# Kernel tuning notes

Hardware: AMD Instinct MI355X
Metric: run time of the kernel (lower is better)

Reference implementation:

```python
import jax, jax.numpy as jnp
import numpy as np

K = 8          # opt.pk, explicit precision cutoff
MARGIN = 0.2   # opt.margin
NEG = -1e30    # sentinel for masked sort keys


def setup_inputs() -> dict:
    key = jax.random.key(0)
    k1, k2 = jax.random.split(key)
    batch_reprs = jax.random.normal(k1, (4096, 512), dtype=jnp.float32)
    batch_labels = jax.random.randint(k2, (4096,), 0, 64)
    return {"batch_reprs": batch_reprs, "batch_labels": batch_labels}


def _forward(batch_reprs, batch_labels):
    B = batch_reprs.shape[0]
    dt = batch_reprs.dtype
    # cls_match_mat: 1 if same class
    match = (batch_labels[:, None] == batch_labels[None, :]).astype(dt)
    # pairwise euclidean distance (squared=False), safe sqrt at zero diagonal
    sq = jnp.sum(batch_reprs * batch_reprs, axis=1)
    res = jnp.maximum(sq[:, None] - 2.0 * (batch_reprs @ batch_reprs.T) + sq[None, :], 0.0)
    zero = res <= 0.0
    d = jnp.where(zero, 0.0, jnp.sqrt(jnp.where(zero, 1.0, res)))
    sim_hat = -d + (1.0 - match) * MARGIN  # use_margin=True path
    # rank via double argsort (descending similarity -> rank 1 = best)
    order = jnp.argsort(-sim_hat, axis=1)
    rank = jnp.argsort(order, axis=1).astype(dt) + 1.0
    pos_nums = jnp.sum(match, axis=1)
    ks = jnp.minimum(pos_nums, jnp.asarray(K + 1, dt))[:, None]  # k_mat per row
    w = 1.0 / jnp.log2(rank + 1.0) + 1.0  # DCG-style rank weight
    # false positives: not same class, within top-k_i
    fp_mask = (match < 1.0) & (rank <= ks)
    fp_nums = jnp.sum(fp_mask, axis=1)  # |N| per row
    # false negatives: same class, beyond top-k_i
    fn_mask = (match > 0.0) & (rank > ks)
    fp_term = jnp.sum(jnp.where(fp_mask, sim_hat * w, 0.0))
    # per-row variable-size topk over false negatives, vectorized:
    # mask non-FN entries to -inf, sort desc, keep first fp_nums[i] entries
    fn_key = jnp.where(fn_mask, sim_hat, NEG)
    fn_order = jnp.argsort(-fn_key, axis=1)
    sorted_sim = jnp.take_along_axis(sim_hat, fn_order, axis=1)
    sorted_w = jnp.take_along_axis(w, fn_order, axis=1)
    sorted_valid = jnp.take_along_axis(fn_mask, fn_order, axis=1)
    take = (jnp.arange(B)[None, :].astype(dt) < fp_nums[:, None]) & sorted_valid
    fn_term = jnp.sum(jnp.where(take, sorted_sim * sorted_w, 0.0))
    # rows with fp_num==0 contribute 0 to both terms, matching the host loop
    return fp_term - fn_term


def reference(batch_reprs, batch_labels):
    return _forward(batch_reprs, batch_labels)
```

## Files before the change

### kernel.cpp

```cpp
#include <hip/hip_runtime.h>
#include <math.h>

#define BB 4096
#define DD 512
#define KTOP 9
#define MARGIN_F 0.2f
#define NT64 64
#define NTRI64 (NT64 * (NT64 + 1) / 2)

typedef __attribute__((ext_vector_type(8))) short short8;
typedef __attribute__((ext_vector_type(4))) float f32x4;
typedef unsigned long long u64;

__device__ unsigned short g_Rhi[(size_t)BB * DD];
__device__ unsigned short g_Rlo[(size_t)BB * DD];
__device__ u64 g_cmask[64 * 64];

__device__ __forceinline__ unsigned short f2bf(float x) {
  unsigned u = __float_as_uint(x);
  u += 0x7fffu + ((u >> 16) & 1u);
  return (unsigned short)(u >> 16);
}
__device__ __forceinline__ float bf2f(unsigned short h) {
  return __uint_as_float((unsigned)h << 16);
}

__device__ __forceinline__ void gload16(void* lds, const void* g) {
  __builtin_amdgcn_global_load_lds(
      (const __attribute__((address_space(1))) void*)g,
      (__attribute__((address_space(3))) void*)lds, 16, 0, 0);
}

#define FENCE() asm volatile("" ::: "memory")

__device__ __forceinline__ float ord16val(unsigned o16) {
  unsigned e = (o16 << 16) | 0x8000u;
  unsigned s = (e & 0x80000000u) ? (e ^ 0x80000000u) : ~e;
  return __uint_as_float(s);
}

__device__ __forceinline__ unsigned wavemax32_dpp(unsigned c) {
#define MSTEP(CTRL, RM)                                                        \
  {                                                                            \
    unsigned o = (unsigned)__builtin_amdgcn_update_dpp(0, (int)c, CTRL, RM, 0xf, false); \
    if (o > c) c = o;                                                          \
  }
  MSTEP(0xB1, 0xf) MSTEP(0x4E, 0xf) MSTEP(0x141, 0xf) MSTEP(0x140, 0xf)
  MSTEP(0x142, 0xa) MSTEP(0x143, 0xc)
#undef MSTEP
  return (unsigned)__builtin_amdgcn_readlane((int)c, 63);
}

__device__ __forceinline__ int wavesum_dpp(int c) {
#define SSTEP(CTRL, RM)                                                        \
  c += __builtin_amdgcn_update_dpp(0, c, CTRL, RM, 0xf, false);
  SSTEP(0xB1, 0xf) SSTEP(0x4E, 0xf) SSTEP(0x141, 0xf) SSTEP(0x140, 0xf)
  SSTEP(0x142, 0xa) SSTEP(0x143, 0xc)
#undef SSTEP
  return __builtin_amdgcn_readlane(c, 63);
}

__device__ __forceinline__ unsigned u4c(const uint4& f, int q) {
  return q == 0 ? f.x : q == 1 ? f.y : q == 2 ? f.z : f.w;
}

__global__ __launch_bounds__(64) void splitsq(const float* __restrict__ R,
                                              float* __restrict__ sq) {
  const int row = blockIdx.x, lane = threadIdx.x;
  const float4* r4 = (const float4*)(R + (size_t)row * DD);
  float4 a = r4[lane], b = r4[lane + 64];
  float xs[8] = {a.x, a.y, a.z, a.w, b.x, b.y, b.z, b.w};
  unsigned short hs[8], ls[8];
  float s = 0.f;
  #pragma unroll
  for (int q = 0; q < 8; ++q) {
    float x = xs[q];
    s += x * x;
    unsigned short hh = f2bf(x);
    hs[q] = hh;
    ls[q] = f2bf(x - bf2f(hh));
  }
  const size_t base = (size_t)row * DD;
  *(ushort4*)&g_Rhi[base + lane * 4]       = *(ushort4*)&hs[0];
  *(ushort4*)&g_Rhi[base + 256 + lane * 4] = *(ushort4*)&hs[4];
  *(ushort4*)&g_Rlo[base + lane * 4]       = *(ushort4*)&ls[0];
  *(ushort4*)&g_Rlo[base + 256 + lane * 4] = *(ushort4*)&ls[4];
  #pragma unroll
  for (int off = 32; off; off >>= 1) s += __shfl_down(s, off);
  if (lane == 0) sq[row] = s;
}

__global__ __launch_bounds__(64) void buildmask(const int* __restrict__ labels) {
  __shared__ int slab[BB];
  const int c = blockIdx.x, lane = threadIdx.x;
  for (int i = lane; i < BB / 4; i += 64) ((int4*)slab)[i] = ((const int4*)labels)[i];
  __syncthreads();
  u64 m = 0;
  #pragma unroll
  for (int e = 0; e < 64; ++e) {
    int j = 512 * (e >> 3) + 8 * lane + (e & 7);
    m |= (u64)(slab[j] == c) << e;
  }
  g_cmask[c * 64 + lane] = m;
}

__global__ __launch_bounds__(256) void simgemm_mfma(const int* __restrict__ labels,
                                                    const float* __restrict__ sq,
                                                    unsigned short* __restrict__ simq) {
  const int x = blockIdx.x & 7;
  int c = blockIdx.x >> 3;
  int bi = 0, bj = 0;
  #pragma unroll
  for (int q = 0; q < 8; ++q) {
    const int bjq = (q < 4) ? (4 * x + q) : (56 - 4 * x + q);
    const int n = bjq + 1;
    if (c >= 0 && c < n) { bj = bjq; bi = c; }
    c -= n;
  }
  const int i0 = bi * 64, j0 = bj * 64;

  __shared__ unsigned short smem[3][3 * 2048];

  const int tid = threadIdx.x;
  const int wid = tid >> 6, lane = tid & 63;
  const int wr = wid >> 1, wc = wid & 1;
  const int lrow = lane & 15, kblk = lane >> 4;

  const int r_a = lane >> 2;
  const int c_sw = (((lane & 3) ^ (r_a & 3)) * 8);

  f32x4 acc[2][2] = {};

  auto stage = [&](unsigned short* buf, int k0) {
    const int r = wid * 16 + r_a;
    const size_t ga = (size_t)(i0 + r) * DD + k0 + c_sw;
    const size_t gb = (size_t)(j0 + r) * DD + k0 + c_sw;
    gload16(&buf[wid * 512],        &g_Rhi[ga]);
    gload16(&buf[2048 + wid * 512], &g_Rhi[gb]);
    gload16(&buf[4096 + wid * 512], &g_Rlo[gb]);
  };

  stage(smem[0], 0);
  stage(smem[1], 32);

  #pragma unroll
  for (int step = 0; step < 16; ++step) {
    if (step + 2 < 16) stage(smem[(step + 2) % 3], (step + 2) * 32);
    if (step < 14)      asm volatile("s_waitcnt vmcnt(6)" ::: "memory");
    else if (step == 14) asm volatile("s_waitcnt vmcnt(3)" ::: "memory");
    else                 asm volatile("s_waitcnt vmcnt(0)" ::: "memory");
    __builtin_amdgcn_s_barrier();
    FENCE();

    unsigned short* sAhi = smem[step % 3];
    unsigned short* sBhi = sAhi + 2048;
    unsigned short* sBlo = sAhi + 4096;

    short8 ah[2], bh[2], bl[2];
    #pragma unroll
    for (int m = 0; m < 2; ++m) {
      const int rr = wr * 32 + m * 16 + lrow;
      const int off = rr * 32 + ((kblk ^ (lrow & 3)) * 8);
      ah[m] = *(const short8*)&sAhi[off];
    }
    #pragma unroll
    for (int n = 0; n < 2; ++n) {
      const int rr = wc * 32 + n * 16 + lrow;
      const int off = rr * 32 + ((kblk ^ (lrow & 3)) * 8);
      bh[n] = *(const short8*)&sBhi[off];
      bl[n] = *(const short8*)&sBlo[off];
    }
    #pragma unroll
    for (int m = 0; m < 2; ++m) {
      #pragma unroll
      for (int n = 0; n < 2; ++n) {
        acc[m][n] = __builtin_amdgcn_mfma_f32_16x16x32_bf16(ah[m], bh[n], acc[m][n], 0, 0, 0);
        acc[m][n] = __builtin_amdgcn_mfma_f32_16x16x32_bf16(ah[m], bl[n], acc[m][n], 0, 0, 0);
      }
    }
    FENCE();
    __builtin_amdgcn_s_barrier();
    FENCE();
  }

  __syncthreads();
  unsigned short (*T)[68] = (unsigned short (*)[68])smem[0];
  float* sqi = (float*)smem[1];
  float* sqj = sqi + 64;
  int* labi = (int*)(sqj + 64);
  int* labj = labi + 64;
  if (tid < 64) { sqi[tid] = sq[i0 + tid]; labi[tid] = labels[i0 + tid]; }
  else if (tid < 128) { int t2 = tid - 64; sqj[t2] = sq[j0 + t2]; labj[t2] = labels[j0 + t2]; }
  __syncthreads();

  #pragma unroll
  for (int m = 0; m < 2; ++m) {
    const int rbase = wr * 32 + m * 16 + kblk * 4;
    #pragma unroll
    for (int n = 0; n < 2; ++n) {
      const int ccol = wc * 32 + n * 16 + lrow;
      const float sqc = sqj[ccol];
      const int lc_ = labj[ccol];
      #pragma unroll
      for (int reg = 0; reg < 4; ++reg) {
        const int r = rbase + reg;
        float res = sqi[r] - 2.0f * acc[m][n][reg] + sqc;
        float dd = (res <= 0.f) ? 0.f : sqrtf(res);
        float sv = -dd + ((labi[r] != lc_) ? MARGIN_F : 0.f);
        unsigned su = __float_as_uint(sv);
        unsigned ord = su ^ ((unsigned)((int)su >> 31) | 0x80000000u);
        T[r][ccol] = (unsigned short)(ord >> 16);
      }
    }
  }
  __syncthreads();

  const bool offdiag = (bi != bj);
  const int row = tid >> 2, seg = tid & 3;
  uint4 w0 = *(const uint4*)&T[row][seg * 16];
  uint4 w1 = *(const uint4*)&T[row][seg * 16 + 8];
  *(uint4*)&simq[(size_t)(i0 + row) * BB + j0 + seg * 16]     = w0;
  *(uint4*)&simq[(size_t)(i0 + row) * BB + j0 + seg * 16 + 8] = w1;
  if (offdiag) {
    unsigned short tmp[16];
    #pragma unroll
    for (int r2 = 0; r2 < 16; ++r2) tmp[r2] = T[seg * 16 + r2][row];
    *(uint4*)&simq[(size_t)(j0 + row) * BB + i0 + seg * 16]     = *(uint4*)&tmp[0];
    *(uint4*)&simq[(size_t)(j0 + row) * BB + i0 + seg * 16 + 8] = *(uint4*)&tmp[8];
  }
}

#define EKEY(e) ((((u4c(v[(e) >> 3], ((e) & 7) >> 1) >> (16 * ((e) & 1))) & 0xffffu) << 13) \
                 | (lbase - (unsigned)((512 * ((e) >> 3) + ((e) & 7)) << 1)                 \
                    + (unsigned)((mask >> (e)) & 1ull)))

#define TOP2UPD(k, a, b) {                                                     \
  unsigned _mx = ((k) > (a)) ? (k) : (a);                                      \
  unsigned _mn = ((k) > (a)) ? (a) : (k);                                      \
  (a) = _mx;                                                                   \
  (b) = (_mn > (b)) ? _mn : (b); }

__global__ __launch_bounds__(256) void rowproc6(const unsigned short* __restrict__ simq,
                                                const int* __restrict__ labels,
                                                float* __restrict__ partials) {
  const int tid = threadIdx.x;
  const int lane = tid & 63;
  const int row = blockIdx.x * 4 + (tid >> 6);

  const uint4* rowp = (const uint4*)(simq + (size_t)row * BB);
  uint4 v[8];
  #pragma unroll
  for (int s = 0; s < 8; ++s) v[s] = rowp[lane + s * 64];

  const int myl = labels[row];
  const u64 mask = g_cmask[myl * 64 + lane];
  const unsigned lbase = (unsigned)((4095 - 8 * lane) << 1);

  unsigned h1 = 0, h2 = 0;
  #pragma unroll
  for (int e = 0; e < 64; ++e) {
    unsigned k = EKEY(e);
    TOP2UPD(k, h1, h2);
  }
  const int pos = wavesum_dpp(__popcll(mask));
  const int ks = min(pos, KTOP);

  unsigned kth = 0;
  float fp = 0.f; int fpn = 0;
  #pragma unroll
  for (int t = 0; t < KTOP; ++t) {
    if (t < ks) {
      unsigned g = wavemax32_dpp(h1);
      if (!(g & 1u)) { fp += ord16val(g >> 13) * (1.f / log2f((float)(t + 2)) + 1.f); fpn++; }
      if (t == ks - 1) kth = g;
      if (h1 == g) {
        h1 = h2; h2 = ~0u;
        if (h1 == ~0u) {
          h1 = 0; h2 = 0;
          #pragma unroll
          for (int e = 0; e < 64; ++e) {
            unsigned k = EKEY(e);
            if (k < g) TOP2UPD(k, h1, h2);
          }
        }
      }
    }
  }

  float fn = 0.f;
  if (fpn > 0) {
    unsigned f1 = 0, f2 = 0;
    #pragma unroll
    for (int e = 0; e < 64; ++e) {
      unsigned k = EKEY(e);
      if ((k & 1u) && k < kth) TOP2UPD(k, f1, f2);
    }
    unsigned ck[KTOP];
    int nc = 0;
    #pragma unroll
    for (int u = 0; u < KTOP; ++u) {
      ck[u] = ~0u;
      if (u < fpn) {
        unsigned g = wavemax32_dpp(f1);
        if (g != 0u) {
          ck[u] = g; nc = u + 1;
          if (f1 == g) {
            f1 = f2; f2 = ~0u;
            if (f1 == ~0u) {
              f1 = 0; f2 = 0;
              #pragma unroll
              for (int e = 0; e < 64; ++e) {
                unsigned k = EKEY(e);
                if ((k & 1u) && k < g) TOP2UPD(k, f1, f2);
              }
            }
          }
        }
      }
    }
    if (nc > 0) {
      int cnt[KTOP];
      #pragma unroll
      for (int u = 0; u < KTOP; ++u) cnt[u] = 0;
      #pragma unroll
      for (int e = 0; e < 64; ++e) {
        unsigned k = EKEY(e);
        #pragma unroll
        for (int u = 0; u < KTOP; ++u) cnt[u] += (k > ck[u]) ? 1 : 0;
      }
      #pragma unroll
      for (int u = 0; u < KTOP; ++u) cnt[u] = wavesum_dpp(cnt[u]);
      #pragma unroll
      for (int u = 0; u < KTOP; ++u) {
        if (u < nc) {
          int rank = 1 + cnt[u];
          fn += ord16val(ck[u] >> 13) * (1.f / log2f((float)(rank + 1)) + 1.f);
        }
      }
    }
  }

  if (lane == 0) partials[row] = fp - fn;
}

__global__ __launch_bounds__(256) void finalreduce(const float* __restrict__ partials,
                                                   float* __restrict__ out) {
  __shared__ float s[256];
  const int tid = threadIdx.x;
  float acc = 0.f;
  for (int j = tid; j < BB; j += 256) acc += partials[j];
  s[tid] = acc; __syncthreads();
  #pragma unroll
  for (int st = 128; st; st >>= 1) { if (tid < st) s[tid] += s[tid + st]; __syncthreads(); }
  if (tid == 0) out[0] = s[0];
}

extern "C" void kernel_launch(void* const* d_in, const int* in_sizes, int n_in,
                              void* d_out, int out_size, void* d_ws, size_t ws_size,
                              hipStream_t stream) {
  const float* R      = (const float*)d_in[0];
  const int*   labels = (const int*)d_in[1];
  float* out = (float*)d_out;

  unsigned short* simq = (unsigned short*)d_ws;
  float* sq            = (float*)((char*)d_ws + (size_t)BB * BB * 2);
  float* partials      = sq + BB;

  splitsq<<<BB, 64, 0, stream>>>(R, sq);
  buildmask<<<64, 64, 0, stream>>>(labels);
  simgemm_mfma<<<NTRI64, 256, 0, stream>>>(labels, sq, simq);
  rowproc6<<<BB / 4, 256, 0, stream>>>(simq, labels, partials);
  finalreduce<<<1, 256, 0, stream>>>(partials, out);
}
```

Baseline: 97.56 us.

## Drop bf16 low-part split GEMM and use single-wave 64x64 tiles

Removes the hi/lo bf16 split of the B operand, so the distance GEMM runs in plain bf16 with half the MFMA work and no g_Rlo writes or reads. The GEMM kernel is rebuilt as one wave per 64x64 tile with a 4x4 accumulator grid, double-buffered LDS loads, and no block barriers. The epilogue transpose and stores are redone for 64 threads. Lower precision can change the similarity ordering near ties and so shift ranks, and fewer threads per block lowers per-block parallelism and epilogue throughput.

```diff
diff --git a/kernel.cpp b/kernel.cpp
--- a/kernel.cpp
+++ b/kernel.cpp
@@ -13,7 +13,6 @@
 typedef unsigned long long u64;
 
 __device__ unsigned short g_Rhi[(size_t)BB * DD];
-__device__ unsigned short g_Rlo[(size_t)BB * DD];
 __device__ u64 g_cmask[64 * 64];
 
 __device__ __forceinline__ unsigned short f2bf(float x) {
@@ -21,17 +20,12 @@
   u += 0x7fffu + ((u >> 16) & 1u);
   return (unsigned short)(u >> 16);
 }
-__device__ __forceinline__ float bf2f(unsigned short h) {
-  return __uint_as_float((unsigned)h << 16);
-}
 
 __device__ __forceinline__ void gload16(void* lds, const void* g) {
   __builtin_amdgcn_global_load_lds(
       (const __attribute__((address_space(1))) void*)g,
       (__attribute__((address_space(3))) void*)lds, 16, 0, 0);
 }
-
-#define FENCE() asm volatile("" ::: "memory")
 
 __device__ __forceinline__ float ord16val(unsigned o16) {
   unsigned e = (o16 << 16) | 0x8000u;
@@ -70,21 +64,17 @@
   const float4* r4 = (const float4*)(R + (size_t)row * DD);
   float4 a = r4[lane], b = r4[lane + 64];
   float xs[8] = {a.x, a.y, a.z, a.w, b.x, b.y, b.z, b.w};
-  unsigned short hs[8], ls[8];
+  unsigned short hs[8];
   float s = 0.f;
   #pragma unroll
   for (int q = 0; q < 8; ++q) {
     float x = xs[q];
     s += x * x;
-    unsigned short hh = f2bf(x);
-    hs[q] = hh;
-    ls[q] = f2bf(x - bf2f(hh));
+    hs[q] = f2bf(x);
   }
   const size_t base = (size_t)row * DD;
   *(ushort4*)&g_Rhi[base + lane * 4]       = *(ushort4*)&hs[0];
   *(ushort4*)&g_Rhi[base + 256 + lane * 4] = *(ushort4*)&hs[4];
-  *(ushort4*)&g_Rlo[base + lane * 4]       = *(ushort4*)&ls[0];
-  *(ushort4*)&g_Rlo[base + 256 + lane * 4] = *(ushort4*)&ls[4];
   #pragma unroll
   for (int off = 32; off; off >>= 1) s += __shfl_down(s, off);
   if (lane == 0) sq[row] = s;
@@ -104,9 +94,9 @@
   g_cmask[c * 64 + lane] = m;
 }
 
-__global__ __launch_bounds__(256) void simgemm_mfma(const int* __restrict__ labels,
-                                                    const float* __restrict__ sq,
-                                                    unsigned short* __restrict__ simq) {
+__global__ __launch_bounds__(64) void simgemm_wave(const int* __restrict__ labels,
+                                                   const float* __restrict__ sq,
+                                                   unsigned short* __restrict__ simq) {
   const int x = blockIdx.x & 7;
   int c = blockIdx.x >> 3;
   int bi = 0, bj = 0;
@@ -119,86 +109,69 @@
   }
   const int i0 = bi * 64, j0 = bj * 64;
 
-  __shared__ unsigned short smem[3][3 * 2048];
-
-  const int tid = threadIdx.x;
-  const int wid = tid >> 6, lane = tid & 63;
-  const int wr = wid >> 1, wc = wid & 1;
+  __shared__ unsigned short smem[2][2][2048];
+
+  const int lane = threadIdx.x;
   const int lrow = lane & 15, kblk = lane >> 4;
 
-  const int r_a = lane >> 2;
-  const int c_sw = (((lane & 3) ^ (r_a & 3)) * 8);
-
-  f32x4 acc[2][2] = {};
-
-  auto stage = [&](unsigned short* buf, int k0) {
-    const int r = wid * 16 + r_a;
-    const size_t ga = (size_t)(i0 + r) * DD + k0 + c_sw;
-    const size_t gb = (size_t)(j0 + r) * DD + k0 + c_sw;
-    gload16(&buf[wid * 512],        &g_Rhi[ga]);
-    gload16(&buf[2048 + wid * 512], &g_Rhi[gb]);
-    gload16(&buf[4096 + wid * 512], &g_Rlo[gb]);
+  f32x4 acc[4][4] = {};
+
+  auto stage = [&](int buf, int k0) {
+    const int sr = lane & 15;
+    const int sc = (lane >> 4) * 8;
+    #pragma unroll
+    for (int m = 0; m < 4; ++m) {
+      gload16(&smem[buf][0][m * 512], &g_Rhi[(size_t)(i0 + m * 16 + sr) * DD + k0 + sc]);
+      gload16(&smem[buf][1][m * 512], &g_Rhi[(size_t)(j0 + m * 16 + sr) * DD + k0 + sc]);
+    }
   };
 
-  stage(smem[0], 0);
-  stage(smem[1], 32);
+  stage(0, 0);
+  stage(1, 32);
 
   #pragma unroll
   for (int step = 0; step < 16; ++step) {
-    if (step + 2 < 16) stage(smem[(step + 2) % 3], (step + 2) * 32);
-    if (step < 14)      asm volatile("s_waitcnt vmcnt(6)" ::: "memory");
-    else if (step == 14) asm volatile("s_waitcnt vmcnt(3)" ::: "memory");
-    else                 asm volatile("s_waitcnt vmcnt(0)" ::: "memory");
-    __builtin_amdgcn_s_barrier();
-    FENCE();
-
-    unsigned short* sAhi = smem[step % 3];
-    unsigned short* sBhi = sAhi + 2048;
-    unsigned short* sBlo = sAhi + 4096;
-
-    short8 ah[2], bh[2], bl[2];
-    #pragma unroll
-    for (int m = 0; m < 2; ++m) {
-      const int rr = wr * 32 + m * 16 + lrow;
-      const int off = rr * 32 + ((kblk ^ (lrow & 3)) * 8);
-      ah[m] = *(const short8*)&sAhi[off];
-    }
-    #pragma unroll
-    for (int n = 0; n < 2; ++n) {
-      const int rr = wc * 32 + n * 16 + lrow;
-      const int off = rr * 32 + ((kblk ^ (lrow & 3)) * 8);
-      bh[n] = *(const short8*)&sBhi[off];
-      bl[n] = *(const short8*)&sBlo[off];
-    }
-    #pragma unroll
-    for (int m = 0; m < 2; ++m) {
-      #pragma unroll
-      for (int n = 0; n < 2; ++n) {
-        acc[m][n] = __builtin_amdgcn_mfma_f32_16x16x32_bf16(ah[m], bh[n], acc[m][n], 0, 0, 0);
-        acc[m][n] = __builtin_amdgcn_mfma_f32_16x16x32_bf16(ah[m], bl[n], acc[m][n], 0, 0, 0);
-      }
-    }
-    FENCE();
-    __builtin_amdgcn_s_barrier();
-    FENCE();
-  }
-
-  __syncthreads();
-  unsigned short (*T)[68] = (unsigned short (*)[68])smem[0];
-  float* sqi = (float*)smem[1];
+    const int cur = step & 1;
+    if (step == 15) asm volatile("s_waitcnt vmcnt(0)" ::: "memory");
+    else            asm volatile("s_waitcnt vmcnt(8)" ::: "memory");
+    __builtin_amdgcn_sched_barrier(0);
+
+    short8 a[4], b[4];
+    #pragma unroll
+    for (int m = 0; m < 4; ++m) a[m] = *(const short8*)&smem[cur][0][m * 512 + lane * 8];
+    #pragma unroll
+    for (int n = 0; n < 4; ++n) b[n] = *(const short8*)&smem[cur][1][n * 512 + lane * 8];
+    asm volatile("s_waitcnt lgkmcnt(0)" ::: "memory");
+    __builtin_amdgcn_sched_barrier(0);
+
+    if (step < 14) stage(cur, (step + 2) * 32);
+
+    #pragma unroll
+    for (int m = 0; m < 4; ++m) {
+      #pragma unroll
+      for (int n = 0; n < 4; ++n) {
+        acc[m][n] = __builtin_amdgcn_mfma_f32_16x16x32_bf16(a[m], b[n], acc[m][n], 0, 0, 0);
+      }
+    }
+  }
+
+  unsigned short* flat = &smem[0][0][0];
+  unsigned short (*T)[68] = (unsigned short (*)[68])flat;
+  float* sqi = (float*)(flat + 4608);
   float* sqj = sqi + 64;
   int* labi = (int*)(sqj + 64);
   int* labj = labi + 64;
-  if (tid < 64) { sqi[tid] = sq[i0 + tid]; labi[tid] = labels[i0 + tid]; }
-  else if (tid < 128) { int t2 = tid - 64; sqj[t2] = sq[j0 + t2]; labj[t2] = labels[j0 + t2]; }
-  __syncthreads();
-
-  #pragma unroll
-  for (int m = 0; m < 2; ++m) {
-    const int rbase = wr * 32 + m * 16 + kblk * 4;
-    #pragma unroll
-    for (int n = 0; n < 2; ++n) {
-      const int ccol = wc * 32 + n * 16 + lrow;
+  sqi[lane] = sq[i0 + lane];
+  sqj[lane] = sq[j0 + lane];
+  labi[lane] = labels[i0 + lane];
+  labj[lane] = labels[j0 + lane];
+
+  #pragma unroll
+  for (int m = 0; m < 4; ++m) {
+    const int rbase = m * 16 + kblk * 4;
+    #pragma unroll
+    for (int n = 0; n < 4; ++n) {
+      const int ccol = n * 16 + lrow;
       const float sqc = sqj[ccol];
       const int lc_ = labj[ccol];
       #pragma unroll
@@ -213,20 +186,24 @@
       }
     }
   }
-  __syncthreads();
-
-  const bool offdiag = (bi != bj);
-  const int row = tid >> 2, seg = tid & 3;
-  uint4 w0 = *(const uint4*)&T[row][seg * 16];
-  uint4 w1 = *(const uint4*)&T[row][seg * 16 + 8];
-  *(uint4*)&simq[(size_t)(i0 + row) * BB + j0 + seg * 16]     = w0;
-  *(uint4*)&simq[(size_t)(i0 + row) * BB + j0 + seg * 16 + 8] = w1;
-  if (offdiag) {
-    unsigned short tmp[16];
-    #pragma unroll
-    for (int r2 = 0; r2 < 16; ++r2) tmp[r2] = T[seg * 16 + r2][row];
-    *(uint4*)&simq[(size_t)(j0 + row) * BB + i0 + seg * 16]     = *(uint4*)&tmp[0];
-    *(uint4*)&simq[(size_t)(j0 + row) * BB + i0 + seg * 16 + 8] = *(uint4*)&tmp[8];
+
+  #pragma unroll
+  for (int s = 0; s < 8; ++s) {
+    const int row = s * 8 + (lane >> 3);
+    const int cs = (lane & 7) * 8;
+    short8 w = *(const short8*)&T[row][cs];
+    *(short8*)&simq[(size_t)(i0 + row) * BB + j0 + cs] = w;
+  }
+  if (bi != bj) {
+    #pragma unroll
+    for (int s = 0; s < 8; ++s) {
+      const int col = s * 8 + (lane >> 3);
+      const int rs = (lane & 7) * 8;
+      unsigned short tmp[8];
+      #pragma unroll
+      for (int t = 0; t < 8; ++t) tmp[t] = T[rs + t][col];
+      *(short8*)&simq[(size_t)(j0 + col) * BB + i0 + rs] = *(short8*)tmp;
+    }
   }
 }
 
@@ -368,7 +345,7 @@
 
   splitsq<<<BB, 64, 0, stream>>>(R, sq);
   buildmask<<<64, 64, 0, stream>>>(labels);
-  simgemm_mfma<<<NTRI64, 256, 0, stream>>>(labels, sq, simq);
+  simgemm_wave<<<NTRI64, 64, 0, stream>>>(labels, sq, simq);
   rowproc6<<<BB / 4, 256, 0, stream>>>(simq, labels, partials);
   finalreduce<<<1, 256, 0, stream>>>(partials, out);
 }
```

After: 96.12 us. No clear change (-1.5%).
